# Optimization experiments

Measured on AMD Instinct MI355X. Metric: run time of the kernel, lower is better.

Reference implementation:

```python
import jax, jax.numpy as jnp
import numpy as np


def _sqdist(X1, X2):
    # squared euclidean distance matrix, matches torch.cdist(...,p=2)**2
    d2 = (jnp.sum(X1 * X1, -1)[:, None] + jnp.sum(X2 * X2, -1)[None, :]
          - 2.0 * (X1 @ X2.T))
    return jnp.maximum(d2, 0.0)


def setup_inputs() -> dict:
    key = jax.random.key(0)
    k1, k2, k3, k4, k5, k6 = jax.random.split(key, 6)
    n, m, d, C = 1024, 2048, 4, 64
    X_train = jax.random.normal(k1, (n, d), dtype=jnp.float32)
    y_train = jax.random.normal(k2, (n,), dtype=jnp.float32)
    X_test = jax.random.normal(k3, (m, d), dtype=jnp.float32)
    # positive params within the priors' supports
    lengthscale = jax.random.uniform(k4, (C,), minval=0.1, maxval=3.0, dtype=jnp.float32)
    variance = jax.random.uniform(k5, (C,), minval=0.1, maxval=3.0, dtype=jnp.float32)
    noise = jax.random.uniform(k6, (C,), minval=0.01, maxval=0.5, dtype=jnp.float32)
    return {"X_train": X_train, "y_train": y_train, "X_test": X_test,
            "lengthscale": lengthscale, "variance": variance, "noise": noise}


def reference(X_train, y_train, X_test, lengthscale, variance, noise):
    n = X_train.shape[0]
    ls2 = (lengthscale ** 2)[:, None, None]          # [C,1,1]
    var = variance[:, None, None]                     # [C,1,1]
    d2_tr = _sqdist(X_train, X_train)                 # [n,n]
    d2_te = _sqdist(X_test, X_train)                  # [m,n]
    K_train = var * jnp.exp(-0.5 * d2_tr[None] / ls2)   # [C,n,n]
    K_test = var * jnp.exp(-0.5 * d2_te[None] / ls2)    # [C,m,n]
    K_noisy = K_train + noise[:, None, None] * jnp.eye(n, dtype=K_train.dtype)
    L = jnp.linalg.cholesky(K_noisy)                  # batched [C,n,n]

    def per_chain(Lc, Ktc):
        solve = jax.scipy.linalg.solve_triangular
        z = solve(Lc, y_train, lower=True)            # [n]
        alpha = solve(Lc, z, lower=True, trans=1)     # [n]
        pred_mean = Ktc @ alpha                       # [m]
        v = solve(Lc, Ktc.T, lower=True)              # [n,m]
        pred_var = jnp.sum(v * v, axis=0)             # [m]
        return pred_mean, pred_var

    means, vars_ = jax.vmap(per_chain)(L, K_test)     # [C,m] each
    return means.mean(axis=0), vars_.mean(axis=0)
```

## Files before the change

### kernel.cpp

```cpp
#include <hip/hip_runtime.h>
#include <math.h>

#define N 1024
#define M 2048
#define C 64
#define NB 128
#define TB 8
#define PAD 4
#define TP 40
#define NBLK 36
#define PL ((size_t)NBLK*NB*NB)

typedef __attribute__((ext_vector_type(8))) short bf16x8;
typedef __attribute__((ext_vector_type(4))) float f32x4;

__device__ __forceinline__ size_t pblk(int ib, int jt){
    return ((size_t)((ib*(ib+1))/2 + jt))*((size_t)NB*NB);
}

#define TT(r,c) T[(r)][(((c)+(r)) & 127)]


__device__ __forceinline__ float sqdist4(const float4 a, const float4 b){
    float dx=a.x-b.x, dy=a.y-b.y, dz=a.z-b.z, dw=a.w-b.w;
    return dx*dx+dy*dy+dz*dz+dw*dw;
}

__device__ __forceinline__ void split4(float x0, float x1, float x2, float x3,
                                       uint2& hi, uint2& lo){
    unsigned b0=__float_as_uint(x0), b1=__float_as_uint(x1),
             b2=__float_as_uint(x2), b3=__float_as_uint(x3);
    unsigned h0=b0&0xFFFF0000u, h1=b1&0xFFFF0000u, h2=b2&0xFFFF0000u, h3=b3&0xFFFF0000u;
    hi.x = (h0>>16)|h1;  hi.y = (h2>>16)|h3;
    float l0=x0-__uint_as_float(h0), l1=x1-__uint_as_float(h1),
          l2=x2-__uint_as_float(h2), l3=x3-__uint_as_float(h3);
    lo.x = (__float_as_uint(l0)>>16) | (__float_as_uint(l1)&0xFFFF0000u);
    lo.y = (__float_as_uint(l2)>>16) | (__float_as_uint(l3)&0xFFFF0000u);
}

__device__ void chol_invert_lds(float T[NB][NB], int tid){
    for (int j = 0; j < NB; j++){
        float d = TT(j,j);
        float inv = 1.0f / sqrtf(d);
        for (int i = j+1+tid; i < NB; i += 256) TT(i,j) *= inv;
        if (tid == 0) TT(j,j) = d * inv;
        __syncthreads();
        int i = j+1 + (tid >> 1);
        if (i < NB){
            float lij = TT(i,j);
            for (int k = j+1+(tid&1); k <= i; k += 2)
                TT(i,k) -= lij * TT(k,j);
        }
        __syncthreads();
    }
    for (int i = 0; i < NB; i++){
        float inv_ii = 1.0f / TT(i,i);
        int j = tid & 127, hi = tid >> 7;
        float S = 0.0f;
        if (j < i){
            for (int k = i-1-hi; k >= j; k -= 2)
                S += TT(i,k) * TT(k,j);
        }
        if (hi && j < i) TT(j,i) = S;
        __syncthreads();
        if (!hi){
            if (j < i)      TT(i,j) = -inv_ii * (S + TT(j,i));
            else if (j == i) TT(i,i) = inv_ii;
        }
        __syncthreads();
    }
}


__device__ __forceinline__ void load_tileT(float Ts[32][NB+PAD], const float* __restrict__ S,
                                           int lds_, int tid){
    int k4 = (tid & 7) * 4, c0 = tid >> 3;
    #pragma unroll
    for (int cc = c0; cc < NB; cc += 32){
        float4 v = *(const float4*)&S[(size_t)cc*lds_ + k4];
        Ts[k4+0][cc] = v.x; Ts[k4+1][cc] = v.y; Ts[k4+2][cc] = v.z; Ts[k4+3][cc] = v.w;
    }
}

__device__ __forceinline__ void load_tileS(float Ts[32][NB+PAD], const float* __restrict__ S,
                                           int lds_, int tid){
    int c4 = (tid & 31) * 4, kk = tid >> 5;
    #pragma unroll
    for (int k = kk; k < 32; k += 8){
        float4 v = *(const float4*)&S[(size_t)k*lds_ + c4];
        *(float4*)&Ts[k][c4] = v;
    }
}

__device__ __forceinline__ void mm32(const float As[32][NB+PAD], const float Bs[32][NB+PAD],
                                     int r0, int ca, int cb, float acc[8][8]){
    #pragma unroll 8
    for (int k = 0; k < 32; k++){
        float4 a0 = *(const float4*)&As[k][r0];
        float4 a1 = *(const float4*)&As[k][r0+4];
        float4 b0 = *(const float4*)&Bs[k][ca];
        float4 b1 = *(const float4*)&Bs[k][cb];
        float a[8] = {a0.x,a0.y,a0.z,a0.w,a1.x,a1.y,a1.z,a1.w};
        float b[8] = {b0.x,b0.y,b0.z,b0.w,b1.x,b1.y,b1.z,b1.w};
        #pragma unroll
        for (int u=0;u<8;u++)
            #pragma unroll
            for (int v=0;v<8;v++)
                acc[u][v] += a[u]*b[v];
    }
}

__device__ __forceinline__ void gemm_core(const float* __restrict__ A, int lda,
                                          const float* __restrict__ B, int ldb,
                                          int klen, bool bT, float acc[8][8],
                                          float As[32][NB+PAD], float Bs[32][NB+PAD])
{
    int tid = threadIdx.x;
    int r0 = (tid >> 4) * 8, ca = (tid & 15) * 4, cb = 64 + ca;
    for (int k0 = 0; k0 < klen; k0 += 32){
        load_tileT(As, A + k0, lda, tid);
        if (bT) load_tileT(Bs, B + k0, ldb, tid);
        else    load_tileS(Bs, B + (size_t)k0*ldb, ldb, tid);
        __syncthreads();
        mm32(As, Bs, r0, ca, cb, acc);
        __syncthreads();
    }
}

__device__ __forceinline__ void store_acc(float* __restrict__ Cp, int ldc,
                                          const float acc[8][8], float sgn){
    int tid = threadIdx.x;
    int r0 = (tid >> 4) * 8, ca = (tid & 15) * 4, cb = 64 + ca;
    #pragma unroll
    for (int u=0;u<8;u++){
        float4 v0 = make_float4(sgn*acc[u][0], sgn*acc[u][1], sgn*acc[u][2], sgn*acc[u][3]);
        float4 v1 = make_float4(sgn*acc[u][4], sgn*acc[u][5], sgn*acc[u][6], sgn*acc[u][7]);
        *(float4*)&Cp[(size_t)(r0+u)*ldc + ca] = v0;
        *(float4*)&Cp[(size_t)(r0+u)*ldc + cb] = v1;
    }
}

struct SmGemm { float As[32][NB+PAD]; float Bs[32][NB+PAD]; };
union SmU { SmGemm g; float T[NB][NB]; };


__global__ void k_init_acc(float* __restrict__ acc){
    int i = blockIdx.x*blockDim.x + threadIdx.x;
    if (i < 2*M) acc[i] = 0.0f;
}

__global__ void k_build_d2te(const float* __restrict__ Xtr, const float* __restrict__ Xte,
                             float* __restrict__ d2){
    int j = blockIdx.x;
    float4 xj = ((const float4*)Xte)[j];
    for (int i = threadIdx.x; i < N; i += blockDim.x){
        float4 xi = ((const float4*)Xtr)[i];
        d2[(size_t)j*N + i] = sqdist4(xi,xj);
    }
}

__global__ __launch_bounds__(256) void k_build_K(const float* __restrict__ Xtr,
                          const float* __restrict__ ls,
                          const float* __restrict__ var, const float* __restrict__ noise,
                          float* __restrict__ Lbuf){
    __shared__ float4 xr[NB], xc[NB];
    int c = blockIdx.y, flat = blockIdx.x;
    int ib = 0; while ((ib+1)*(ib+2)/2 <= flat) ib++;
    int jt = flat - ib*(ib+1)/2;
    int tid = threadIdx.x;
    if (tid < NB) xr[tid] = ((const float4*)Xtr)[ib*NB + tid];
    else          xc[tid-NB] = ((const float4*)Xtr)[jt*NB + (tid-NB)];
    __syncthreads();
    float il2 = 1.0f/(ls[c]*ls[c]);
    float vc = var[c], nc = noise[c];
    float* blk = Lbuf + c*PL + pblk(ib,jt);
    for (int idx = tid; idx < NB*NB; idx += 256){
        int r = idx >> 7, col = idx & 127;
        float d2v = sqdist4(xr[r], xc[col]);
        float v = vc*__expf(-0.5f*d2v*il2);
        if (ib==jt && r==col) v += nc;
        blk[idx] = v;
    }
}

__global__ __launch_bounds__(256) void k_diagF(float* __restrict__ Lbuf){
    __shared__ float T[NB][NB];
    int c = blockIdx.x, tid = threadIdx.x;
    float* A = Lbuf + c*PL + pblk(0,0);
    for (int idx = tid; idx < NB*NB; idx += 256){
        int r = idx >> 7, col = idx & 127;
        TT(r,col) = A[idx];
    }
    __syncthreads();
    chol_invert_lds(T, tid);
    for (int idx = tid; idx < NB*NB; idx += 256){
        int r = idx >> 7, col = idx & 127;
        A[idx] = (col <= r) ? TT(r,col) : 0.0f;
    }
}

__global__ __launch_bounds__(256) void k_panel(float* __restrict__ Lbuf, int kb){
    __shared__ float As[32][NB+PAD];
    __shared__ float Bs[32][NB+PAD];
    int c = blockIdx.x;
    int ib = kb + 1 + blockIdx.y;
    float* base = Lbuf + c*PL;
    float* Ablk = base + pblk(ib,kb);
    const float* Dv = base + pblk(kb,kb);
    float acc[8][8] = {};
    gemm_core(Ablk, NB, Dv, NB, NB, true, acc, As, Bs);
    store_acc(Ablk, NB, acc, 1.0f);
}

__global__ __launch_bounds__(256) void k_syrk(float* __restrict__ Lbuf, int kb){
    __shared__ SmU sm;
    int c = blockIdx.x;
    int flat = blockIdx.y;
    int di = 0; while ((di+1)*(di+2)/2 <= flat) di++;
    int dj = flat - di*(di+1)/2;
    int i = kb+1+di, j = kb+1+dj;
    float* base = Lbuf + c*PL;
    float* Cblk = base + pblk(i,j);
    const float* Ablk = base + pblk(i,kb);
    const float* Bblk = base + pblk(j,kb);
    float acc[8][8] = {};
    gemm_core(Ablk, NB, Bblk, NB, NB, true, acc, sm.g.As, sm.g.Bs);
    int tid = threadIdx.x;
    int r0 = (tid >> 4) * 8, ca = (tid & 15) * 4, cb = 64 + ca;
    if (flat != 0){
        #pragma unroll
        for (int u=0;u<8;u++){
            float4 c0v = *(float4*)&Cblk[(size_t)(r0+u)*NB + ca];
            float4 c1v = *(float4*)&Cblk[(size_t)(r0+u)*NB + cb];
            c0v.x -= acc[u][0]; c0v.y -= acc[u][1]; c0v.z -= acc[u][2]; c0v.w -= acc[u][3];
            c1v.x -= acc[u][4]; c1v.y -= acc[u][5]; c1v.z -= acc[u][6]; c1v.w -= acc[u][7];
            *(float4*)&Cblk[(size_t)(r0+u)*NB + ca] = c0v;
            *(float4*)&Cblk[(size_t)(r0+u)*NB + cb] = c1v;
        }
    } else {
        float (*T)[NB] = sm.T;
        #pragma unroll
        for (int u=0;u<8;u++){
            float4 c0v = *(const float4*)&Cblk[(size_t)(r0+u)*NB + ca];
            float4 c1v = *(const float4*)&Cblk[(size_t)(r0+u)*NB + cb];
            TT(r0+u, ca+0) = c0v.x - acc[u][0];
            TT(r0+u, ca+1) = c0v.y - acc[u][1];
            TT(r0+u, ca+2) = c0v.z - acc[u][2];
            TT(r0+u, ca+3) = c0v.w - acc[u][3];
            TT(r0+u, cb+0) = c1v.x - acc[u][4];
            TT(r0+u, cb+1) = c1v.y - acc[u][5];
            TT(r0+u, cb+2) = c1v.z - acc[u][6];
            TT(r0+u, cb+3) = c1v.w - acc[u][7];
        }
        __syncthreads();
        chol_invert_lds(T, tid);
        for (int idx = tid; idx < NB*NB; idx += 256){
            int r = idx >> 7, col = idx & 127;
            Cblk[idx] = (col <= r) ? TT(r,col) : 0.0f;
        }
    }
}

__global__ __launch_bounds__(256) void k_gemmA(float* __restrict__ Trow,
                                               const float* __restrict__ Lbuf, int ib){
    __shared__ float As[32][NB+PAD];
    __shared__ float Bs[32][NB+PAD];
    int c = blockIdx.x, ct = blockIdx.y;
    const float* base = Lbuf + c*PL;
    const float* Dv = base + pblk(ib,ib);
    const float* Bsrc = base + pblk(ib,ct);
    float acc[8][8] = {};
    gemm_core(Dv, NB, Bsrc, NB, NB, false, acc, As, Bs);
    store_acc(Trow + (size_t)c*NB*N + ct*NB, N, acc, 1.0f);
}

__global__ __launch_bounds__(256) void k_gemmB(float* __restrict__ Lbuf,
                                               const float* __restrict__ Trow, int ib){
    __shared__ float As[32][NB+PAD];
    __shared__ float Bs[32][NB+PAD];
    int c = blockIdx.x, jt = blockIdx.y;
    const float* G = Trow + (size_t)c*NB*N;
    float* base = Lbuf + c*PL;
    float acc[8][8] = {};
    for (int kt = jt; kt < ib; kt++)
        gemm_core(G + kt*NB, N, base + pblk(kt,jt), NB, NB, false, acc, As, Bs);
    store_acc(base + pblk(ib,jt), NB, acc, -1.0f);
}

__global__ void k_zvec(const float* __restrict__ Lbuf, const float* __restrict__ y,
                       float* __restrict__ z){
    int c = blockIdx.x;
    int p = blockIdx.y * 4 + (threadIdx.x >> 6);
    int lane = threadIdx.x & 63;
    int pb = p >> 7, pl = p & 127;
    const float* base = Lbuf + c*PL;
    float s = 0.0f;
    for (int kt = 0; kt <= pb; kt++){
        const float* row = base + pblk(pb,kt) + (size_t)pl*NB;
        int lim = (kt==pb) ? pl : NB-1;
        for (int i = lane; i <= lim; i += 64) s += row[i]*y[kt*NB + i];
    }
    for (int off = 32; off; off >>= 1) s += __shfl_down(s, off);
    if (lane == 0) z[c*N + p] = s;
}

__global__ __launch_bounds__(256) void k_bigg(const float* __restrict__ Lbuf,
                                              const float* __restrict__ d2,
                                              const float* __restrict__ zbuf,
                                              const float* __restrict__ ls,
                                              const float* __restrict__ var,
                                              float* __restrict__ acc_out){
    __shared__ unsigned short Ah[NB][TP], Al[NB][TP], Bh[NB][TP], Bl[NB][TP];
    int jt = blockIdx.x, pt = blockIdx.y, c = blockIdx.z;
    int tid = threadIdx.x;
    int lane = tid & 63, w = tid >> 6;
    int wrow = w >> 1, wcol = w & 1;
    float il2 = 1.0f/(ls[c]*ls[c]);
    float vc = var[c];
    float ec = -0.5f*il2;
    const float* Arow = d2 + (size_t)(jt*NB)*N;
    const float* Wbase = Lbuf + c*PL;
    int klen = (pt+1)*NB;
    f32x4 acc[4][4];
    #pragma unroll
    for (int i=0;i<4;i++)
        #pragma unroll
        for (int j=0;j<4;j++) acc[i][j] = (f32x4)0.0f;

    int q = tid & 7, rs = tid >> 3;
    int fr = lane & 15, kg = lane >> 4;
    int ar = wrow*64 + fr, br = wcol*64 + fr;
    int kc = kg * 8;

    for (int k0 = 0; k0 < klen; k0 += 32){
        const float* Bp = Wbase + pblk(pt, k0 >> 7);
        int kloc = k0 & 127;
        __syncthreads();
        #pragma unroll
        for (int p = 0; p < 4; p++){
            int r = rs + 32*p;
            float4 dv = *(const float4*)&Arow[(size_t)r*N + k0 + q*4];
            float x0 = vc*__expf(ec*dv.x), x1 = vc*__expf(ec*dv.y);
            float x2 = vc*__expf(ec*dv.z), x3 = vc*__expf(ec*dv.w);
            uint2 hi, lo; split4(x0,x1,x2,x3, hi, lo);
            *(uint2*)&Ah[r][q*4] = hi;
            *(uint2*)&Al[r][q*4] = lo;
        }
        #pragma unroll
        for (int p = 0; p < 4; p++){
            int r = rs + 32*p;
            float4 wv = *(const float4*)&Bp[(size_t)r*NB + kloc + q*4];
            uint2 hi, lo; split4(wv.x,wv.y,wv.z,wv.w, hi, lo);
            *(uint2*)&Bh[r][q*4] = hi;
            *(uint2*)&Bl[r][q*4] = lo;
        }
        __syncthreads();
        bf16x8 ah[4], al[4];
        #pragma unroll
        for (int rt=0;rt<4;rt++){
            ah[rt] = *(const bf16x8*)&Ah[ar + rt*16][kc];
            al[rt] = *(const bf16x8*)&Al[ar + rt*16][kc];
        }
        #pragma unroll
        for (int ct=0;ct<4;ct++){
            bf16x8 bh = *(const bf16x8*)&Bh[br + ct*16][kc];
            bf16x8 bl = *(const bf16x8*)&Bl[br + ct*16][kc];
            #pragma unroll
            for (int rt=0;rt<4;rt++){
                f32x4 a = acc[rt][ct];
                a = __builtin_amdgcn_mfma_f32_16x16x32_bf16(ah[rt], bh, a, 0,0,0);
                a = __builtin_amdgcn_mfma_f32_16x16x32_bf16(ah[rt], bl, a, 0,0,0);
                a = __builtin_amdgcn_mfma_f32_16x16x32_bf16(al[rt], bh, a, 0,0,0);
                acc[rt][ct] = a;
            }
        }
    }
    float zv[4];
    #pragma unroll
    for (int ct=0;ct<4;ct++) zv[ct] = zbuf[c*N + pt*NB + wcol*64 + ct*16 + fr];
    #pragma unroll
    for (int rt=0;rt<4;rt++){
        #pragma unroll
        for (int r=0;r<4;r++){
            float m = 0.0f, v = 0.0f;
            #pragma unroll
            for (int ct=0;ct<4;ct++){
                float x = acc[rt][ct][r];
                v += x*x; m += x*zv[ct];
            }
            m += __shfl_xor(m, 1);  v += __shfl_xor(v, 1);
            m += __shfl_xor(m, 2);  v += __shfl_xor(v, 2);
            m += __shfl_xor(m, 4);  v += __shfl_xor(v, 4);
            m += __shfl_xor(m, 8);  v += __shfl_xor(v, 8);
            if (fr == 0){
                int j = jt*NB + wrow*64 + rt*16 + kg*4 + r;
                atomicAdd(&acc_out[j], m);
                atomicAdd(&acc_out[M + j], v);
            }
        }
    }
}

__global__ void k_final(const float* __restrict__ acc, float* __restrict__ out){
    int i = blockIdx.x*blockDim.x + threadIdx.x;
    if (i < 2*M) out[i] = acc[i] * (1.0f/64.0f);
}


extern "C" void kernel_launch(void* const* d_in, const int* in_sizes, int n_in,
                              void* d_out, int out_size, void* d_ws, size_t ws_size,
                              hipStream_t stream) {
    const float* Xtr = (const float*)d_in[0];
    const float* ytr = (const float*)d_in[1];
    const float* Xte = (const float*)d_in[2];
    const float* ls  = (const float*)d_in[3];
    const float* var = (const float*)d_in[4];
    const float* noi = (const float*)d_in[5];
    float* out = (float*)d_out;

    float* ws = (float*)d_ws;
    const size_t shared_fl  = (size_t)N*M + 2*M;
    const size_t perchain   = PL + (size_t)NB*N + (size_t)N;
    size_t avail = ws_size / sizeof(float);
    if (avail < shared_fl + perchain) return;
    int Gmax = (int)((avail - shared_fl) / perchain);
    if (Gmax > C) Gmax = C;
    int nbatch = (C + Gmax - 1) / Gmax;
    int G = (C + nbatch - 1) / nbatch;

    float* d2te = ws;
    float* acc  = d2te + (size_t)N*M;
    float* Lbuf = acc  + 2*M;
    float* Trow = Lbuf + (size_t)G*PL;
    float* zbuf = Trow + (size_t)G*NB*N;

    k_init_acc<<<dim3((2*M+255)/256), dim3(256), 0, stream>>>(acc);
    k_build_d2te<<<dim3(M), dim3(256), 0, stream>>>(Xtr, Xte, d2te);

    for (int c0 = 0; c0 < C; c0 += G){
        int g = C - c0 < G ? C - c0 : G;

        k_build_K<<<dim3(NBLK, g), dim3(256), 0, stream>>>(Xtr, ls+c0, var+c0, noi+c0, Lbuf);
        k_diagF<<<dim3(g), dim3(256), 0, stream>>>(Lbuf);

        for (int kb = 0; kb < TB-1; kb++){
            int rem = TB-1-kb;
            k_panel<<<dim3(g, rem), dim3(256), 0, stream>>>(Lbuf, kb);
            k_syrk<<<dim3(g, rem*(rem+1)/2), dim3(256), 0, stream>>>(Lbuf, kb);
        }
        for (int ib = 1; ib < TB; ib++){
            k_gemmA<<<dim3(g, ib), dim3(256), 0, stream>>>(Trow, Lbuf, ib);
            k_gemmB<<<dim3(g, ib), dim3(256), 0, stream>>>(Lbuf, Trow, ib);
        }
        k_zvec<<<dim3(g, N/4), dim3(256), 0, stream>>>(Lbuf, ytr, zbuf);
        k_bigg<<<dim3(M/NB, TB, g), dim3(256), 0, stream>>>(Lbuf, d2te, zbuf, ls+c0, var+c0, acc);
    }
    k_final<<<dim3((2*M+255)/256), dim3(256), 0, stream>>>(acc, out);
}
```

Baseline: 6.213 ms.

## Move blocked Cholesky GEMMs to split-f16 MFMA and fragment-ordered LDS

Replaces the scalar FP32 8x8 register-tile GEMM used in the panel, SYRK and inverse-multiply kernels with a split-precision f16 (hi+lo, three MFMAs) matrix-core path. Operand tiles are staged into LDS in MFMA fragment order, so each lane reads one contiguous 16-byte vector. The big prediction GEMM gets the same fragment-ordered layout. This aims to cut the FP32 ALU cost of the factorization. It risks accuracy loss inside the Cholesky, where f16 range and split error can amplify, and the strided non-contiguous loads and scalar stores may be uncoalesced.

```diff
diff --git a/kernel.cpp b/kernel.cpp
--- a/kernel.cpp
+++ b/kernel.cpp
@@ -1,4 +1,5 @@
 #include <hip/hip_runtime.h>
+#include <hip/hip_fp16.h>
 #include <math.h>
 
 #define N 1024
@@ -6,12 +7,11 @@
 #define C 64
 #define NB 128
 #define TB 8
-#define PAD 4
-#define TP 40
 #define NBLK 36
 #define PL ((size_t)NBLK*NB*NB)
 
 typedef __attribute__((ext_vector_type(8))) short bf16x8;
+typedef __attribute__((ext_vector_type(8))) _Float16 f16x8;
 typedef __attribute__((ext_vector_type(4))) float f32x4;
 
 __device__ __forceinline__ size_t pblk(int ib, int jt){
@@ -72,76 +72,94 @@
 }
 
 
-__device__ __forceinline__ void load_tileT(float Ts[32][NB+PAD], const float* __restrict__ S,
-                                           int lds_, int tid){
-    int k4 = (tid & 7) * 4, c0 = tid >> 3;
-    #pragma unroll
-    for (int cc = c0; cc < NB; cc += 32){
-        float4 v = *(const float4*)&S[(size_t)cc*lds_ + k4];
-        Ts[k4+0][cc] = v.x; Ts[k4+1][cc] = v.y; Ts[k4+2][cc] = v.z; Ts[k4+3][cc] = v.w;
-    }
-}
-
-__device__ __forceinline__ void load_tileS(float Ts[32][NB+PAD], const float* __restrict__ S,
-                                           int lds_, int tid){
-    int c4 = (tid & 31) * 4, kk = tid >> 5;
-    #pragma unroll
-    for (int k = kk; k < 32; k += 8){
-        float4 v = *(const float4*)&S[(size_t)k*lds_ + c4];
-        *(float4*)&Ts[k][c4] = v;
-    }
-}
-
-__device__ __forceinline__ void mm32(const float As[32][NB+PAD], const float Bs[32][NB+PAD],
-                                     int r0, int ca, int cb, float acc[8][8]){
-    #pragma unroll 8
-    for (int k = 0; k < 32; k++){
-        float4 a0 = *(const float4*)&As[k][r0];
-        float4 a1 = *(const float4*)&As[k][r0+4];
-        float4 b0 = *(const float4*)&Bs[k][ca];
-        float4 b1 = *(const float4*)&Bs[k][cb];
-        float a[8] = {a0.x,a0.y,a0.z,a0.w,a1.x,a1.y,a1.z,a1.w};
-        float b[8] = {b0.x,b0.y,b0.z,b0.w,b1.x,b1.y,b1.z,b1.w};
-        #pragma unroll
-        for (int u=0;u<8;u++)
+struct FragLds { __half Ah[4096], Al[4096], Bh[4096], Bl[4096]; };
+
+__device__ __forceinline__ void stage_f16(__half* __restrict__ Hh, __half* __restrict__ Hl,
+                                          const float* __restrict__ S, int ld,
+                                          int k0, bool contig, int tid){
+    #pragma unroll
+    for (int h = 0; h < 2; h++){
+        int u = tid + h*256;
+        int fr = u & 15, kg = (u>>4)&3, rt = (u>>6)&3, hf = u>>8;
+        int rc = hf*64 + rt*16 + fr;
+        int kk = k0 + kg*8;
+        float x[8];
+        if (contig){
+            float4 v0 = *(const float4*)&S[(size_t)rc*ld + kk];
+            float4 v1 = *(const float4*)&S[(size_t)rc*ld + kk + 4];
+            x[0]=v0.x;x[1]=v0.y;x[2]=v0.z;x[3]=v0.w;
+            x[4]=v1.x;x[5]=v1.y;x[6]=v1.z;x[7]=v1.w;
+        } else {
             #pragma unroll
-            for (int v=0;v<8;v++)
-                acc[u][v] += a[u]*b[v];
-    }
-}
-
-__device__ __forceinline__ void gemm_core(const float* __restrict__ A, int lda,
-                                          const float* __restrict__ B, int ldb,
-                                          int klen, bool bT, float acc[8][8],
-                                          float As[32][NB+PAD], float Bs[32][NB+PAD])
-{
-    int tid = threadIdx.x;
-    int r0 = (tid >> 4) * 8, ca = (tid & 15) * 4, cb = 64 + ca;
-    for (int k0 = 0; k0 < klen; k0 += 32){
-        load_tileT(As, A + k0, lda, tid);
-        if (bT) load_tileT(Bs, B + k0, ldb, tid);
-        else    load_tileS(Bs, B + (size_t)k0*ldb, ldb, tid);
-        __syncthreads();
-        mm32(As, Bs, r0, ca, cb, acc);
-        __syncthreads();
-    }
-}
-
-__device__ __forceinline__ void store_acc(float* __restrict__ Cp, int ldc,
-                                          const float acc[8][8], float sgn){
-    int tid = threadIdx.x;
-    int r0 = (tid >> 4) * 8, ca = (tid & 15) * 4, cb = 64 + ca;
-    #pragma unroll
-    for (int u=0;u<8;u++){
-        float4 v0 = make_float4(sgn*acc[u][0], sgn*acc[u][1], sgn*acc[u][2], sgn*acc[u][3]);
-        float4 v1 = make_float4(sgn*acc[u][4], sgn*acc[u][5], sgn*acc[u][6], sgn*acc[u][7]);
-        *(float4*)&Cp[(size_t)(r0+u)*ldc + ca] = v0;
-        *(float4*)&Cp[(size_t)(r0+u)*ldc + cb] = v1;
-    }
-}
-
-struct SmGemm { float As[32][NB+PAD]; float Bs[32][NB+PAD]; };
-union SmU { SmGemm g; float T[NB][NB]; };
+            for (int e=0;e<8;e++) x[e] = S[(size_t)(kk+e)*ld + rc];
+        }
+        union { __half h[8]; uint4 u4; } Hi, Lo;
+        #pragma unroll
+        for (int e=0;e<8;e++){
+            __half hv = __float2half_rn(x[e]);
+            Hi.h[e] = hv;
+            Lo.h[e] = __float2half_rn(x[e] - __half2float(hv));
+        }
+        *(uint4*)&Hh[(size_t)u*8] = Hi.u4;
+        *(uint4*)&Hl[(size_t)u*8] = Lo.u4;
+    }
+}
+
+__device__ __forceinline__ void mfma_slab_f16(const __half* Ah, const __half* Al,
+                                              const __half* Bh, const __half* Bl,
+                                              int wrow, int wcol, int lane,
+                                              f32x4 acc[4][4]){
+    f16x8 ah[4], al[4];
+    #pragma unroll
+    for (int rt=0;rt<4;rt++){
+        ah[rt] = *(const f16x8*)&Ah[((size_t)((wrow*4+rt)*64 + lane))*8];
+        al[rt] = *(const f16x8*)&Al[((size_t)((wrow*4+rt)*64 + lane))*8];
+    }
+    #pragma unroll
+    for (int ct=0;ct<4;ct++){
+        f16x8 bh = *(const f16x8*)&Bh[((size_t)((wcol*4+ct)*64 + lane))*8];
+        f16x8 bl = *(const f16x8*)&Bl[((size_t)((wcol*4+ct)*64 + lane))*8];
+        #pragma unroll
+        for (int rt=0;rt<4;rt++){
+            f32x4 a = acc[rt][ct];
+            a = __builtin_amdgcn_mfma_f32_16x16x32_f16(ah[rt], bh, a, 0,0,0);
+            a = __builtin_amdgcn_mfma_f32_16x16x32_f16(ah[rt], bl, a, 0,0,0);
+            a = __builtin_amdgcn_mfma_f32_16x16x32_f16(al[rt], bh, a, 0,0,0);
+            acc[rt][ct] = a;
+        }
+    }
+}
+
+__device__ void gemm_f16_unit(const float* __restrict__ A, int lda,
+                              const float* __restrict__ B, int ldb, bool bContig,
+                              FragLds& F, f32x4 acc[4][4], int tid){
+    int lane = tid & 63, w = tid >> 6, wrow = w>>1, wcol = w&1;
+    for (int k0 = 0; k0 < NB; k0 += 32){
+        __syncthreads();
+        stage_f16(F.Ah, F.Al, A, lda, k0, true, tid);
+        stage_f16(F.Bh, F.Bl, B, ldb, k0, bContig, tid);
+        __syncthreads();
+        mfma_slab_f16(F.Ah, F.Al, F.Bh, F.Bl, wrow, wcol, lane, acc);
+    }
+}
+
+__device__ __forceinline__ void store_f16acc(float* __restrict__ Cp, int ldc,
+                                             const f32x4 acc[4][4], float sgn, int tid){
+    int lane = tid&63, w = tid>>6, wrow = w>>1, wcol = w&1;
+    int fr = lane&15, kg = lane>>4;
+    #pragma unroll
+    for (int rt=0;rt<4;rt++)
+      #pragma unroll
+      for (int ct=0;ct<4;ct++)
+        #pragma unroll
+        for (int r=0;r<4;r++){
+            int row = wrow*64 + rt*16 + kg*4 + r;
+            int col = wcol*64 + ct*16 + fr;
+            Cp[(size_t)row*ldc + col] = sgn*acc[rt][ct][r];
+        }
+}
+
+#define ZERO_ACC(acc) { _Pragma("unroll") for (int zi=0;zi<4;zi++) _Pragma("unroll") for (int zj=0;zj<4;zj++) acc[zi][zj] = (f32x4)0.0f; }
 
 
 __global__ void k_init_acc(float* __restrict__ acc){
@@ -200,58 +218,59 @@
 }
 
 __global__ __launch_bounds__(256) void k_panel(float* __restrict__ Lbuf, int kb){
-    __shared__ float As[32][NB+PAD];
-    __shared__ float Bs[32][NB+PAD];
+    __shared__ FragLds F;
     int c = blockIdx.x;
     int ib = kb + 1 + blockIdx.y;
+    int tid = threadIdx.x;
     float* base = Lbuf + c*PL;
     float* Ablk = base + pblk(ib,kb);
     const float* Dv = base + pblk(kb,kb);
-    float acc[8][8] = {};
-    gemm_core(Ablk, NB, Dv, NB, NB, true, acc, As, Bs);
-    store_acc(Ablk, NB, acc, 1.0f);
-}
-
+    f32x4 acc[4][4]; ZERO_ACC(acc);
+    gemm_f16_unit(Ablk, NB, Dv, NB, true, F, acc, tid);
+    store_f16acc(Ablk, NB, acc, 1.0f, tid);
+}
+
+union SmU2 { FragLds f; float T[NB][NB]; };
 __global__ __launch_bounds__(256) void k_syrk(float* __restrict__ Lbuf, int kb){
-    __shared__ SmU sm;
+    __shared__ SmU2 sm;
     int c = blockIdx.x;
     int flat = blockIdx.y;
     int di = 0; while ((di+1)*(di+2)/2 <= flat) di++;
     int dj = flat - di*(di+1)/2;
     int i = kb+1+di, j = kb+1+dj;
+    int tid = threadIdx.x;
     float* base = Lbuf + c*PL;
     float* Cblk = base + pblk(i,j);
     const float* Ablk = base + pblk(i,kb);
     const float* Bblk = base + pblk(j,kb);
-    float acc[8][8] = {};
-    gemm_core(Ablk, NB, Bblk, NB, NB, true, acc, sm.g.As, sm.g.Bs);
-    int tid = threadIdx.x;
-    int r0 = (tid >> 4) * 8, ca = (tid & 15) * 4, cb = 64 + ca;
+    f32x4 acc[4][4]; ZERO_ACC(acc);
+    gemm_f16_unit(Ablk, NB, Bblk, NB, true, sm.f, acc, tid);
+    int lane = tid&63, w = tid>>6, wrow = w>>1, wcol = w&1;
+    int fr = lane&15, kg = lane>>4;
     if (flat != 0){
         #pragma unroll
-        for (int u=0;u<8;u++){
-            float4 c0v = *(float4*)&Cblk[(size_t)(r0+u)*NB + ca];
-            float4 c1v = *(float4*)&Cblk[(size_t)(r0+u)*NB + cb];
-            c0v.x -= acc[u][0]; c0v.y -= acc[u][1]; c0v.z -= acc[u][2]; c0v.w -= acc[u][3];
-            c1v.x -= acc[u][4]; c1v.y -= acc[u][5]; c1v.z -= acc[u][6]; c1v.w -= acc[u][7];
-            *(float4*)&Cblk[(size_t)(r0+u)*NB + ca] = c0v;
-            *(float4*)&Cblk[(size_t)(r0+u)*NB + cb] = c1v;
-        }
+        for (int rt=0;rt<4;rt++)
+          #pragma unroll
+          for (int ct=0;ct<4;ct++)
+            #pragma unroll
+            for (int r=0;r<4;r++){
+                int row = wrow*64 + rt*16 + kg*4 + r;
+                int col = wcol*64 + ct*16 + fr;
+                Cblk[(size_t)row*NB + col] -= acc[rt][ct][r];
+            }
     } else {
+        __syncthreads();
         float (*T)[NB] = sm.T;
         #pragma unroll
-        for (int u=0;u<8;u++){
-            float4 c0v = *(const float4*)&Cblk[(size_t)(r0+u)*NB + ca];
-            float4 c1v = *(const float4*)&Cblk[(size_t)(r0+u)*NB + cb];
-            TT(r0+u, ca+0) = c0v.x - acc[u][0];
-            TT(r0+u, ca+1) = c0v.y - acc[u][1];
-            TT(r0+u, ca+2) = c0v.z - acc[u][2];
-            TT(r0+u, ca+3) = c0v.w - acc[u][3];
-            TT(r0+u, cb+0) = c1v.x - acc[u][4];
-            TT(r0+u, cb+1) = c1v.y - acc[u][5];
-            TT(r0+u, cb+2) = c1v.z - acc[u][6];
-            TT(r0+u, cb+3) = c1v.w - acc[u][7];
-        }
+        for (int rt=0;rt<4;rt++)
+          #pragma unroll
+          for (int ct=0;ct<4;ct++)
+            #pragma unroll
+            for (int r=0;r<4;r++){
+                int row = wrow*64 + rt*16 + kg*4 + r;
+                int col = wcol*64 + ct*16 + fr;
+                TT(row,col) = Cblk[(size_t)row*NB + col] - acc[rt][ct][r];
+            }
         __syncthreads();
         chol_invert_lds(T, tid);
         for (int idx = tid; idx < NB*NB; idx += 256){
@@ -263,28 +282,28 @@
 
 __global__ __launch_bounds__(256) void k_gemmA(float* __restrict__ Trow,
                                                const float* __restrict__ Lbuf, int ib){
-    __shared__ float As[32][NB+PAD];
-    __shared__ float Bs[32][NB+PAD];
+    __shared__ FragLds F;
     int c = blockIdx.x, ct = blockIdx.y;
+    int tid = threadIdx.x;
     const float* base = Lbuf + c*PL;
     const float* Dv = base + pblk(ib,ib);
     const float* Bsrc = base + pblk(ib,ct);
-    float acc[8][8] = {};
-    gemm_core(Dv, NB, Bsrc, NB, NB, false, acc, As, Bs);
-    store_acc(Trow + (size_t)c*NB*N + ct*NB, N, acc, 1.0f);
+    f32x4 acc[4][4]; ZERO_ACC(acc);
+    gemm_f16_unit(Dv, NB, Bsrc, NB, false, F, acc, tid);
+    store_f16acc(Trow + (size_t)c*NB*N + ct*NB, N, acc, 1.0f, tid);
 }
 
 __global__ __launch_bounds__(256) void k_gemmB(float* __restrict__ Lbuf,
                                                const float* __restrict__ Trow, int ib){
-    __shared__ float As[32][NB+PAD];
-    __shared__ float Bs[32][NB+PAD];
+    __shared__ FragLds F;
     int c = blockIdx.x, jt = blockIdx.y;
+    int tid = threadIdx.x;
     const float* G = Trow + (size_t)c*NB*N;
     float* base = Lbuf + c*PL;
-    float acc[8][8] = {};
+    f32x4 acc[4][4]; ZERO_ACC(acc);
     for (int kt = jt; kt < ib; kt++)
-        gemm_core(G + kt*NB, N, base + pblk(kt,jt), NB, NB, false, acc, As, Bs);
-    store_acc(base + pblk(ib,jt), NB, acc, -1.0f);
+        gemm_f16_unit(G + kt*NB, N, base + pblk(kt,jt), NB, false, F, acc, tid);
+    store_f16acc(base + pblk(ib,jt), NB, acc, -1.0f, tid);
 }
 
 __global__ void k_zvec(const float* __restrict__ Lbuf, const float* __restrict__ y,
@@ -310,7 +329,7 @@
                                               const float* __restrict__ ls,
                                               const float* __restrict__ var,
                                               float* __restrict__ acc_out){
-    __shared__ unsigned short Ah[NB][TP], Al[NB][TP], Bh[NB][TP], Bl[NB][TP];
+    __shared__ unsigned short Ah[4096], Al[4096], Bh[4096], Bl[4096];
     int jt = blockIdx.x, pt = blockIdx.y, c = blockIdx.z;
     int tid = threadIdx.x;
     int lane = tid & 63, w = tid >> 6;
@@ -321,50 +340,57 @@
     const float* Arow = d2 + (size_t)(jt*NB)*N;
     const float* Wbase = Lbuf + c*PL;
     int klen = (pt+1)*NB;
-    f32x4 acc[4][4];
-    #pragma unroll
-    for (int i=0;i<4;i++)
-        #pragma unroll
-        for (int j=0;j<4;j++) acc[i][j] = (f32x4)0.0f;
-
-    int q = tid & 7, rs = tid >> 3;
+    f32x4 acc[4][4]; ZERO_ACC(acc);
+
     int fr = lane & 15, kg = lane >> 4;
-    int ar = wrow*64 + fr, br = wcol*64 + fr;
-    int kc = kg * 8;
 
     for (int k0 = 0; k0 < klen; k0 += 32){
         const float* Bp = Wbase + pblk(pt, k0 >> 7);
         int kloc = k0 & 127;
         __syncthreads();
         #pragma unroll
-        for (int p = 0; p < 4; p++){
-            int r = rs + 32*p;
-            float4 dv = *(const float4*)&Arow[(size_t)r*N + k0 + q*4];
-            float x0 = vc*__expf(ec*dv.x), x1 = vc*__expf(ec*dv.y);
-            float x2 = vc*__expf(ec*dv.z), x3 = vc*__expf(ec*dv.w);
-            uint2 hi, lo; split4(x0,x1,x2,x3, hi, lo);
-            *(uint2*)&Ah[r][q*4] = hi;
-            *(uint2*)&Al[r][q*4] = lo;
-        }
-        #pragma unroll
-        for (int p = 0; p < 4; p++){
-            int r = rs + 32*p;
-            float4 wv = *(const float4*)&Bp[(size_t)r*NB + kloc + q*4];
-            uint2 hi, lo; split4(wv.x,wv.y,wv.z,wv.w, hi, lo);
-            *(uint2*)&Bh[r][q*4] = hi;
-            *(uint2*)&Bl[r][q*4] = lo;
+        for (int h = 0; h < 2; h++){
+            int u = tid + h*256;
+            int ufr = u & 15, ukg = (u>>4)&3, urt = (u>>6)&3, uhf = u>>8;
+            int row = uhf*64 + urt*16 + ufr;
+            int kk = k0 + ukg*8;
+            float4 d0 = *(const float4*)&Arow[(size_t)row*N + kk];
+            float4 d1 = *(const float4*)&Arow[(size_t)row*N + kk + 4];
+            float x0 = vc*__expf(ec*d0.x), x1 = vc*__expf(ec*d0.y);
+            float x2 = vc*__expf(ec*d0.z), x3 = vc*__expf(ec*d0.w);
+            float x4 = vc*__expf(ec*d1.x), x5 = vc*__expf(ec*d1.y);
+            float x6 = vc*__expf(ec*d1.z), x7 = vc*__expf(ec*d1.w);
+            uint2 h0, l0, h1, l1;
+            split4(x0,x1,x2,x3, h0, l0);
+            split4(x4,x5,x6,x7, h1, l1);
+            *(uint4*)&Ah[(size_t)u*8] = make_uint4(h0.x,h0.y,h1.x,h1.y);
+            *(uint4*)&Al[(size_t)u*8] = make_uint4(l0.x,l0.y,l1.x,l1.y);
+        }
+        #pragma unroll
+        for (int h = 0; h < 2; h++){
+            int u = tid + h*256;
+            int ufr = u & 15, ukg = (u>>4)&3, urt = (u>>6)&3, uhf = u>>8;
+            int p = uhf*64 + urt*16 + ufr;
+            int kk = kloc + ukg*8;
+            float4 w0 = *(const float4*)&Bp[(size_t)p*NB + kk];
+            float4 w1 = *(const float4*)&Bp[(size_t)p*NB + kk + 4];
+            uint2 h0, l0, h1, l1;
+            split4(w0.x,w0.y,w0.z,w0.w, h0, l0);
+            split4(w1.x,w1.y,w1.z,w1.w, h1, l1);
+            *(uint4*)&Bh[(size_t)u*8] = make_uint4(h0.x,h0.y,h1.x,h1.y);
+            *(uint4*)&Bl[(size_t)u*8] = make_uint4(l0.x,l0.y,l1.x,l1.y);
         }
         __syncthreads();
         bf16x8 ah[4], al[4];
         #pragma unroll
         for (int rt=0;rt<4;rt++){
-            ah[rt] = *(const bf16x8*)&Ah[ar + rt*16][kc];
-            al[rt] = *(const bf16x8*)&Al[ar + rt*16][kc];
+            ah[rt] = *(const bf16x8*)&Ah[((size_t)((wrow*4+rt)*64 + lane))*8];
+            al[rt] = *(const bf16x8*)&Al[((size_t)((wrow*4+rt)*64 + lane))*8];
         }
         #pragma unroll
         for (int ct=0;ct<4;ct++){
-            bf16x8 bh = *(const bf16x8*)&Bh[br + ct*16][kc];
-            bf16x8 bl = *(const bf16x8*)&Bl[br + ct*16][kc];
+            bf16x8 bh = *(const bf16x8*)&Bh[((size_t)((wcol*4+ct)*64 + lane))*8];
+            bf16x8 bl = *(const bf16x8*)&Bl[((size_t)((wcol*4+ct)*64 + lane))*8];
             #pragma unroll
             for (int rt=0;rt<4;rt++){
                 f32x4 a = acc[rt][ct];
```

After: 5.541 ms. -10.8%, faster.
